# Kernel optimization log

Hardware: AMD Instinct MI355X
Metric: run time of the kernel (lower is better)

The kernel has to match this reference:

```python
import jax, jax.numpy as jnp
import numpy as np

DIM = 128          # per-stream channels (init arg `dim`)
C = 2 * DIM        # fused channels
NH = 8             # num_heads
HD = C // NH       # head_dim = 32
K = 3              # kernel_size
DIL = (2, 3)       # dilation list
ND = len(DIL)
SCALE = HD ** -0.5


def setup_inputs() -> dict:
    key = jax.random.key(0)
    ks = jax.random.split(key, 4)
    B, H, W = 4, 80, 80
    rgb = jax.random.normal(ks[0], (B, DIM, H, W), jnp.float32)
    ir = jax.random.normal(ks[1], (B, DIM, H, W), jnp.float32)
    w_qkv = jax.random.normal(ks[2], (3 * C, C), jnp.float32) * (C ** -0.5)
    w_proj = jax.random.normal(ks[3], (C, C), jnp.float32) * (C ** -0.5)
    b_proj = jnp.zeros((C,), jnp.float32)
    return {"rgb": rgb, "ir": ir, "w_qkv": w_qkv, "w_proj": w_proj, "b_proj": b_proj}


def _unfold(x, k, d):
    # nn.Unfold(k, dilation=d, padding=d*(k-1)//2, stride=1) -> [B, c, k*k, H, W]
    B, c, H, W = x.shape
    p = d * (k - 1) // 2
    xp = jnp.pad(x, ((0, 0), (0, 0), (p, p), (p, p)))
    pats = [xp[:, :, i * d:i * d + H, j * d:j * d + W]
            for i in range(k) for j in range(k)]
    return jnp.stack(pats, axis=2)


def _dilate_attention(q, k, v, d):
    # q,k,v: [B, c, H, W] with c = C // ND; attention over k*k dilated neighborhood
    B, c, H, W = q.shape
    h = c // HD
    N = H * W
    qr = q.reshape(B, h, HD, N)                      # [B,h,hd,N]
    ku = _unfold(k, K, d).reshape(B, h, HD, K * K, N)  # [B,h,hd,K2,N]
    vu = _unfold(v, K, d).reshape(B, h, HD, K * K, N)
    attn = jnp.einsum('bhdn,bhdkn->bhnk', qr, ku) * SCALE   # [B,h,N,K2]
    attn = jax.nn.softmax(attn, axis=-1)
    out = jnp.einsum('bhnk,bhdkn->bnhd', attn, vu)          # head-major channels
    return out.reshape(B, H, W, c)


def reference(rgb, ir, w_qkv, w_proj, b_proj):
    y = jnp.concatenate([rgb, ir], axis=1)            # [B, C, H, W]
    B, Cc, H, W = y.shape
    # 1x1 conv qkv, then split channels as [3, num_dilation, C//num_dilation]
    qkv = jnp.einsum('bchw,oc->bohw', y, w_qkv).reshape(B, 3, ND, Cc // ND, H, W)
    outs = [_dilate_attention(qkv[:, 0, i], qkv[:, 1, i], qkv[:, 2, i], DIL[i])
            for i in range(ND)]
    x = jnp.concatenate(outs, axis=-1)                # [B, H, W, C], dilation-major
    x = x @ w_proj.T + b_proj                         # proj Linear(C, C)
    # residual: add rgb to first half of channels, ir to second half
    return x + y.transpose(0, 2, 3, 1)
```

## Files before the change

### kernel.cpp

```cpp
#include <hip/hip_runtime.h>

#define HH 80
#define WW 80
#define NPIX 6400
#define NB 4
#define BN 25600
#define CDIM 256
#define QKVC 768
#define SCALE 0.17677669529663689f

typedef __attribute__((ext_vector_type(8))) short short8;
typedef __attribute__((ext_vector_type(4))) float floatx4;

__device__ __forceinline__ float b2f(ushort u) {
    return __uint_as_float(((uint)u) << 16);
}
__device__ __forceinline__ ushort f2b(float f) {
    uint u = __float_as_uint(f);
    return (ushort)((u + 0x7fffu + ((u >> 16) & 1u)) >> 16);
}
__device__ __forceinline__ void unpack8(uint4 v, float* f) {
    f[0] = __uint_as_float(v.x << 16); f[1] = __uint_as_float(v.x & 0xffff0000u);
    f[2] = __uint_as_float(v.y << 16); f[3] = __uint_as_float(v.y & 0xffff0000u);
    f[4] = __uint_as_float(v.z << 16); f[5] = __uint_as_float(v.z & 0xffff0000u);
    f[6] = __uint_as_float(v.w << 16); f[7] = __uint_as_float(v.w & 0xffff0000u);
}
__device__ __forceinline__ void gload_lds16(const void* gptr, void* lptr) {
    __builtin_amdgcn_global_load_lds(
        (const __attribute__((address_space(1))) unsigned int*)gptr,
        (__attribute__((address_space(3))) unsigned int*)lptr,
        16, 0, 0);
}

__global__ __launch_bounds__(256) void cast_all_k(
    const float* __restrict__ rgb, const float* __restrict__ ir,
    const float* __restrict__ wq, const float* __restrict__ wp,
    ushort* __restrict__ Yb, ushort* __restrict__ wqb, ushort* __restrict__ wpb)
{
    const int tid = threadIdx.x;
    if (blockIdx.x >= 100) {
        int i = (((blockIdx.x - 100) * 8 + blockIdx.y) * 4 + blockIdx.z) * 256 + tid;
        if (i < QKVC * CDIM) wqb[i] = f2b(wq[i]);
        else                 wpb[i - QKVC * CDIM] = f2b(wp[i - QKVC * CDIM]);
        return;
    }
    __shared__ ushort T[32][72];
    const int pix0 = blockIdx.x * 64;
    const int cb = blockIdx.y;
    const int b = blockIdx.z;

    const int pl = tid & 63, cg = tid >> 6;
    #pragma unroll
    for (int cc = 0; cc < 32; cc += 4) {
        int c = cb * 32 + cc + cg;
        const float* src = (c < 128) ? (rgb + ((size_t)b * 128 + c) * NPIX)
                                     : (ir + ((size_t)b * 128 + (c - 128)) * NPIX);
        T[cc + cg][pl] = f2b(src[pix0 + pl]);
    }
    __syncthreads();
    const int nl = tid >> 2, c0 = (tid & 3) * 8;
    ushort tmp[8];
    #pragma unroll
    for (int j = 0; j < 8; ++j) tmp[j] = T[c0 + j][nl];
    uint4 v;
    v.x = tmp[0] | ((uint)tmp[1] << 16);
    v.y = tmp[2] | ((uint)tmp[3] << 16);
    v.z = tmp[4] | ((uint)tmp[5] << 16);
    v.w = tmp[6] | ((uint)tmp[7] << 16);
    *(uint4*)(&Yb[((size_t)(b * NPIX + pix0 + nl)) * CDIM + cb * 32 + c0]) = v;
}

__device__ __forceinline__ void gemm_nt_body64(
    const ushort* __restrict__ A, const ushort* __restrict__ W,
    ushort* As, ushort* Bs, int n0, int o0, floatx4 acc[4][4])
{
    const int tid = threadIdx.x;
    const int lane = tid & 63;
    const int wave = tid >> 6;
    const int wr = wave >> 1, wc = wave & 1;
    const int l15 = lane & 15, quad = lane >> 4;

    const int srow8 = tid >> 3;
    const int scol  = ((tid & 7) * 8) ^ ((srow8 & 1) << 5);
    const int par   = l15 & 1;

    for (int k0 = 0; k0 < CDIM; k0 += 64) {
        #pragma unroll
        for (int r = 0; r < 4; ++r) {
            const int row = r * 32 + srow8;
            gload_lds16(&A[(size_t)(n0 + row) * CDIM + k0 + scol],
                        As + r * 2048 + wave * 512);
            gload_lds16(&W[(size_t)(o0 + row) * CDIM + k0 + scol],
                        Bs + r * 2048 + wave * 512);
        }
        __syncthreads();
        #pragma unroll
        for (int s = 0; s < 2; ++s) {
            const int fc = ((s ^ par) << 5) + quad * 8;
            short8 af[4], bfr[4];
            #pragma unroll
            for (int i = 0; i < 4; ++i)
                af[i] = *(const short8*)(&As[(wr * 64 + i * 16 + l15) * 64 + fc]);
            #pragma unroll
            for (int j = 0; j < 4; ++j)
                bfr[j] = *(const short8*)(&Bs[(wc * 64 + j * 16 + l15) * 64 + fc]);
            #pragma unroll
            for (int i = 0; i < 4; ++i)
                #pragma unroll
                for (int j = 0; j < 4; ++j)
                    acc[i][j] = __builtin_amdgcn_mfma_f32_16x16x32_bf16(
                        bfr[j], af[i], acc[i][j], 0, 0, 0);
        }
        __syncthreads();
    }
}

__global__ __launch_bounds__(256) void gemm_qkv_mfma(
    const ushort* __restrict__ Yb, const ushort* __restrict__ Wb,
    ushort* __restrict__ qkv2)
{
    __shared__ __align__(16) ushort As[128 * 64];
    __shared__ __align__(16) ushort Bs[128 * 64];
    const int tid = threadIdx.x;
    const int lane = tid & 63;
    const int wave = tid >> 6;
    const int wr = wave >> 1, wc = wave & 1;
    const int l15 = lane & 15, quad = lane >> 4;

    const int bid = blockIdx.x;
    const int swz = (bid & 7) * 150 + (bid >> 3);
    const int n0 = (swz / 6) * 128;
    const int o0 = (swz % 6) * 128;

    floatx4 acc[4][4] = {};
    gemm_nt_body64(Yb, Wb, As, Bs, n0, o0, acc);

    #pragma unroll
    for (int i = 0; i < 4; ++i) {
        const int n = n0 + wr * 64 + i * 16 + l15;
        #pragma unroll
        for (int j = 0; j < 4; ++j) {
            const int o4 = o0 + wc * 64 + j * 16 + quad * 4;
            uint2 v;
            v.x = f2b(acc[i][j][0]) | ((uint)f2b(acc[i][j][1]) << 16);
            v.y = f2b(acc[i][j][2]) | ((uint)f2b(acc[i][j][3]) << 16);
            *(uint2*)(qkv2 + (size_t)(o4 >> 5) * BN * 32 + (size_t)n * 32 + (o4 & 31)) = v;
        }
    }
}

template<int D, bool EDGE>
__device__ __forceinline__ void attn_tile(
    const ushort* __restrict__ qkv2, ushort* __restrict__ X2,
    ushort* kl, int b, int dh, int y0, int x0)
{
    constexpr int RW = 16 + 2 * D;
    constexpr int RP = RW * RW;
    const int tid = threadIdx.x;
    const int lane = tid & 63;
    const int wave = tid >> 6;
    const ushort* Qc = qkv2 + (size_t)dh * BN * 32;
    const ushort* Kc = qkv2 + (size_t)(8 + dh) * BN * 32;
    const ushort* Vc = qkv2 + (size_t)(16 + dh) * BN * 32;

    const int px = tid & 15, py = tid >> 4;
    const int n = b * NPIX + (y0 + py) * WW + (x0 + px);
    float q[32];
    {
        const uint4* qp = (const uint4*)(Qc + (size_t)n * 32);
        uint4 v0 = qp[0], v1 = qp[1], v2 = qp[2], v3 = qp[3];
        unpack8(v0, q); unpack8(v1, q + 8); unpack8(v2, q + 16); unpack8(v3, q + 24);
    }

    #pragma unroll 2
    for (int p0 = 0; p0 < RP; p0 += 64) {
        int p = p0 + lane;
        int ry = p / RW, rx = p % RW;
        int gy = y0 - D + ry, gx = x0 - D + rx;
        if (EDGE) { gy = min(max(gy, 0), HH - 1); gx = min(max(gx, 0), WW - 1); }
        if (p < RP)
            gload_lds16(Kc + (size_t)(b * NPIX + gy * WW + gx) * 32 + wave * 8,
                        kl + (size_t)(wave * RP + p0) * 8);
    }
    __syncthreads();

    float sc[9];
    #pragma unroll
    for (int t = 0; t < 9; ++t) {
        const int dy = t / 3 - 1, dx = t % 3 - 1;
        const int p = (py + D + dy * D) * RW + (px + D + dx * D);
        float s = 0.f;
        bool ok = true;
        if (EDGE) {
            const int yy = y0 + py + dy * D, xx = x0 + px + dx * D;
            ok = (yy >= 0 && yy < HH && xx >= 0 && xx < WW);
        }
        if (ok) {
            #pragma unroll
            for (int c = 0; c < 4; ++c) {
                float kv[8];
                unpack8(*(const uint4*)(kl + (size_t)(c * RP + p) * 8), kv);
                #pragma unroll
                for (int j = 0; j < 8; ++j) s += q[c * 8 + j] * kv[j];
            }
        }
        sc[t] = s * SCALE;
    }
    __syncthreads();

    #pragma unroll 2
    for (int p0 = 0; p0 < RP; p0 += 64) {
        int p = p0 + lane;
        int ry = p / RW, rx = p % RW;
        int gy = y0 - D + ry, gx = x0 - D + rx;
        if (EDGE) { gy = min(max(gy, 0), HH - 1); gx = min(max(gx, 0), WW - 1); }
        if (p < RP)
            gload_lds16(Vc + (size_t)(b * NPIX + gy * WW + gx) * 32 + wave * 8,
                        kl + (size_t)(wave * RP + p0) * 8);
    }

    float m = sc[0];
    #pragma unroll
    for (int t = 1; t < 9; ++t) m = fmaxf(m, sc[t]);
    float sum = 0.f;
    #pragma unroll
    for (int t = 0; t < 9; ++t) { sc[t] = __expf(sc[t] - m); sum += sc[t]; }
    const float inv = 1.f / sum;
    __syncthreads();

    float o[32];
    #pragma unroll
    for (int hd = 0; hd < 32; ++hd) o[hd] = 0.f;
    #pragma unroll
    for (int t = 0; t < 9; ++t) {
        const int dy = t / 3 - 1, dx = t % 3 - 1;
        const int p = (py + D + dy * D) * RW + (px + D + dx * D);
        bool ok = true;
        if (EDGE) {
            const int yy = y0 + py + dy * D, xx = x0 + px + dx * D;
            ok = (yy >= 0 && yy < HH && xx >= 0 && xx < WW);
        }
        if (ok) {
            const float wgt = sc[t] * inv;
            #pragma unroll
            for (int c = 0; c < 4; ++c) {
                float vv[8];
                unpack8(*(const uint4*)(kl + (size_t)(c * RP + p) * 8), vv);
                #pragma unroll
                for (int j = 0; j < 8; ++j) o[c * 8 + j] += wgt * vv[j];
            }
        }
    }
    uint4* xp = (uint4*)(X2 + (size_t)dh * BN * 32 + (size_t)n * 32);
    #pragma unroll
    for (int m4 = 0; m4 < 4; ++m4) {
        uint4 v;
        v.x = f2b(o[8 * m4 + 0]) | ((uint)f2b(o[8 * m4 + 1]) << 16);
        v.y = f2b(o[8 * m4 + 2]) | ((uint)f2b(o[8 * m4 + 3]) << 16);
        v.z = f2b(o[8 * m4 + 4]) | ((uint)f2b(o[8 * m4 + 5]) << 16);
        v.w = f2b(o[8 * m4 + 6]) | ((uint)f2b(o[8 * m4 + 7]) << 16);
        xp[m4] = v;
    }
}

__global__ __launch_bounds__(256) void attn2_k(
    const ushort* __restrict__ qkv2, ushort* __restrict__ X2)
{
    __shared__ __align__(16) ushort kl[4 * 484 * 8];
    const int tile = blockIdx.x;
    const int y0 = (tile / 5) * 16, x0 = (tile % 5) * 16;
    const int dh = blockIdx.y;
    const int b = blockIdx.z;
    const bool inter = (y0 >= 16 && y0 <= 48 && x0 >= 16 && x0 <= 48);
    if (dh < 4) {
        if (inter) attn_tile<2, false>(qkv2, X2, kl, b, dh, y0, x0);
        else       attn_tile<2, true >(qkv2, X2, kl, b, dh, y0, x0);
    } else {
        if (inter) attn_tile<3, false>(qkv2, X2, kl, b, dh, y0, x0);
        else       attn_tile<3, true >(qkv2, X2, kl, b, dh, y0, x0);
    }
}

__global__ __launch_bounds__(256) void proj_mfma(
    const ushort* __restrict__ X2, const ushort* __restrict__ Wpb,
    const float* __restrict__ bp, const ushort* __restrict__ Yb,
    float* __restrict__ out)
{
    __shared__ __align__(16) ushort As[64 * 64];
    __shared__ __align__(16) ushort Bs[128 * 64];
    const int tid = threadIdx.x;
    const int lane = tid & 63;
    const int wave = tid >> 6;
    const int wr = wave >> 1, wc = wave & 1;
    const int l15 = lane & 15, quad = lane >> 4;

    const int bid = blockIdx.x;
    const int swz = (bid & 7) * 100 + (bid >> 3);
    const int n0 = (swz >> 1) * 64;
    const int o0 = (swz & 1) * 128;

    const int srow8 = tid >> 3;
    const int scol  = ((tid & 7) * 8) ^ ((srow8 & 1) << 5);
    const int chunk_sel = ((tid >> 2) & 1) ^ (srow8 & 1);
    const int coff  = (tid & 3) * 8;
    const int par   = l15 & 1;

    floatx4 acc[2][4] = {};

    for (int k0 = 0; k0 < CDIM; k0 += 64) {
        const int cbase = k0 >> 5;
        const ushort* Achunk = X2 + (size_t)(cbase + chunk_sel) * BN * 32;
        #pragma unroll
        for (int r = 0; r < 2; ++r) {
            const int row = r * 32 + srow8;
            gload_lds16(&Achunk[(size_t)(n0 + row) * 32 + coff],
                        As + r * 2048 + wave * 512);
        }
        #pragma unroll
        for (int r = 0; r < 4; ++r) {
            const int row = r * 32 + srow8;
            gload_lds16(&Wpb[(size_t)(o0 + row) * CDIM + k0 + scol],
                        Bs + r * 2048 + wave * 512);
        }
        __syncthreads();
        #pragma unroll
        for (int s = 0; s < 2; ++s) {
            const int fc = ((s ^ par) << 5) + quad * 8;
            short8 af[2], bfr[4];
            #pragma unroll
            for (int i = 0; i < 2; ++i)
                af[i] = *(const short8*)(&As[(wr * 32 + i * 16 + l15) * 64 + fc]);
            #pragma unroll
            for (int j = 0; j < 4; ++j)
                bfr[j] = *(const short8*)(&Bs[(wc * 64 + j * 16 + l15) * 64 + fc]);
            #pragma unroll
            for (int i = 0; i < 2; ++i)
                #pragma unroll
                for (int j = 0; j < 4; ++j)
                    acc[i][j] = __builtin_amdgcn_mfma_f32_16x16x32_bf16(
                        bfr[j], af[i], acc[i][j], 0, 0, 0);
        }
        __syncthreads();
    }

    #pragma unroll
    for (int i = 0; i < 2; ++i) {
        const int n = n0 + wr * 32 + i * 16 + l15;
        #pragma unroll
        for (int j = 0; j < 4; ++j) {
            const int o4 = o0 + wc * 64 + j * 16 + quad * 4;
            const float4 bias = *(const float4*)(bp + o4);
            const ushort4 res = *(const ushort4*)(Yb + (size_t)n * CDIM + o4);
            float4 v;
            v.x = acc[i][j][0] + bias.x + b2f(res.x);
            v.y = acc[i][j][1] + bias.y + b2f(res.y);
            v.z = acc[i][j][2] + bias.z + b2f(res.z);
            v.w = acc[i][j][3] + bias.w + b2f(res.w);
            *(float4*)(out + (size_t)n * CDIM + o4) = v;
        }
    }
}

extern "C" void kernel_launch(void* const* d_in, const int* in_sizes, int n_in,
                              void* d_out, int out_size, void* d_ws, size_t ws_size,
                              hipStream_t stream) {
    const float* rgb    = (const float*)d_in[0];
    const float* ir     = (const float*)d_in[1];
    const float* w_qkv  = (const float*)d_in[2];
    const float* w_proj = (const float*)d_in[3];
    const float* b_proj = (const float*)d_in[4];
    float* out = (float*)d_out;

    ushort* qkv2 = (ushort*)d_ws;
    ushort* Yb   = qkv2 + (size_t)24 * BN * 32;
    ushort* X2   = Yb + (size_t)BN * CDIM;
    ushort* Wqb  = X2 + (size_t)8 * BN * 32;
    ushort* Wpb  = Wqb + (size_t)QKVC * CDIM;

    cast_all_k<<<dim3(132, 8, NB), 256, 0, stream>>>(rgb, ir, w_qkv, w_proj,
                                                     Yb, Wqb, Wpb);
    gemm_qkv_mfma<<<dim3(1200), 256, 0, stream>>>(Yb, Wqb, qkv2);
    attn2_k<<<dim3(25, 8, NB), 256, 0, stream>>>(qkv2, X2);
    proj_mfma<<<dim3(800), 256, 0, stream>>>(X2, Wpb, b_proj, Yb, out);
}
```

Baseline: 135.6 us.

## Replace LDS halo staging in attention with direct per-pixel global loads

The attention kernel no longer stages K and V halo tiles into shared memory with barriers. Each thread now reads its nine neighbour K and V vectors straight from global memory and relies on the cache for reuse. The grid is also flattened so that the eight dilation-heads of a tile run in consecutive blocks, which should improve L2 locality. This drops the barriers and LDS traffic and should let more blocks fit per CU, at the cost of redundant global and cache reads.

```diff
diff --git a/kernel.cpp b/kernel.cpp
--- a/kernel.cpp
+++ b/kernel.cpp
@@ -150,21 +150,18 @@
 }
 
 template<int D, bool EDGE>
-__device__ __forceinline__ void attn_tile(
+__device__ __forceinline__ void attn_px(
     const ushort* __restrict__ qkv2, ushort* __restrict__ X2,
-    ushort* kl, int b, int dh, int y0, int x0)
-{
-    constexpr int RW = 16 + 2 * D;
-    constexpr int RP = RW * RW;
-    const int tid = threadIdx.x;
-    const int lane = tid & 63;
-    const int wave = tid >> 6;
+    int b, int dh, int y0, int x0)
+{
+    const int tid = threadIdx.x;
+    const int px = tid & 15, py = tid >> 4;
+    const int yy0 = y0 + py, xx0 = x0 + px;
+    const int n = b * NPIX + yy0 * WW + xx0;
     const ushort* Qc = qkv2 + (size_t)dh * BN * 32;
     const ushort* Kc = qkv2 + (size_t)(8 + dh) * BN * 32;
     const ushort* Vc = qkv2 + (size_t)(16 + dh) * BN * 32;
 
-    const int px = tid & 15, py = tid >> 4;
-    const int n = b * NPIX + (y0 + py) * WW + (x0 + px);
     float q[32];
     {
         const uint4* qp = (const uint4*)(Qc + (size_t)n * 32);
@@ -172,51 +169,25 @@
         unpack8(v0, q); unpack8(v1, q + 8); unpack8(v2, q + 16); unpack8(v3, q + 24);
     }
 
-    #pragma unroll 2
-    for (int p0 = 0; p0 < RP; p0 += 64) {
-        int p = p0 + lane;
-        int ry = p / RW, rx = p % RW;
-        int gy = y0 - D + ry, gx = x0 - D + rx;
-        if (EDGE) { gy = min(max(gy, 0), HH - 1); gx = min(max(gx, 0), WW - 1); }
-        if (p < RP)
-            gload_lds16(Kc + (size_t)(b * NPIX + gy * WW + gx) * 32 + wave * 8,
-                        kl + (size_t)(wave * RP + p0) * 8);
-    }
-    __syncthreads();
-
     float sc[9];
     #pragma unroll
     for (int t = 0; t < 9; ++t) {
         const int dy = t / 3 - 1, dx = t % 3 - 1;
-        const int p = (py + D + dy * D) * RW + (px + D + dx * D);
-        float s = 0.f;
+        int yy = yy0 + dy * D, xx = xx0 + dx * D;
         bool ok = true;
         if (EDGE) {
-            const int yy = y0 + py + dy * D, xx = x0 + px + dx * D;
             ok = (yy >= 0 && yy < HH && xx >= 0 && xx < WW);
-        }
-        if (ok) {
-            #pragma unroll
-            for (int c = 0; c < 4; ++c) {
-                float kv[8];
-                unpack8(*(const uint4*)(kl + (size_t)(c * RP + p) * 8), kv);
-                #pragma unroll
-                for (int j = 0; j < 8; ++j) s += q[c * 8 + j] * kv[j];
-            }
-        }
-        sc[t] = s * SCALE;
-    }
-    __syncthreads();
-
-    #pragma unroll 2
-    for (int p0 = 0; p0 < RP; p0 += 64) {
-        int p = p0 + lane;
-        int ry = p / RW, rx = p % RW;
-        int gy = y0 - D + ry, gx = x0 - D + rx;
-        if (EDGE) { gy = min(max(gy, 0), HH - 1); gx = min(max(gx, 0), WW - 1); }
-        if (p < RP)
-            gload_lds16(Vc + (size_t)(b * NPIX + gy * WW + gx) * 32 + wave * 8,
-                        kl + (size_t)(wave * RP + p0) * 8);
+            yy = min(max(yy, 0), HH - 1);
+            xx = min(max(xx, 0), WW - 1);
+        }
+        const uint4* kp = (const uint4*)(Kc + (size_t)(b * NPIX + yy * WW + xx) * 32);
+        uint4 k0 = kp[0], k1 = kp[1], k2 = kp[2], k3 = kp[3];
+        float kv[32];
+        unpack8(k0, kv); unpack8(k1, kv + 8); unpack8(k2, kv + 16); unpack8(k3, kv + 24);
+        float s = 0.f;
+        #pragma unroll
+        for (int j = 0; j < 32; ++j) s += q[j] * kv[j];
+        sc[t] = (EDGE && !ok) ? 0.f : s * SCALE;
     }
 
     float m = sc[0];
@@ -226,31 +197,29 @@
     #pragma unroll
     for (int t = 0; t < 9; ++t) { sc[t] = __expf(sc[t] - m); sum += sc[t]; }
     const float inv = 1.f / sum;
-    __syncthreads();
 
     float o[32];
     #pragma unroll
-    for (int hd = 0; hd < 32; ++hd) o[hd] = 0.f;
+    for (int j = 0; j < 32; ++j) o[j] = 0.f;
     #pragma unroll
     for (int t = 0; t < 9; ++t) {
         const int dy = t / 3 - 1, dx = t % 3 - 1;
-        const int p = (py + D + dy * D) * RW + (px + D + dx * D);
+        int yy = yy0 + dy * D, xx = xx0 + dx * D;
         bool ok = true;
         if (EDGE) {
-            const int yy = y0 + py + dy * D, xx = x0 + px + dx * D;
             ok = (yy >= 0 && yy < HH && xx >= 0 && xx < WW);
-        }
-        if (ok) {
-            const float wgt = sc[t] * inv;
-            #pragma unroll
-            for (int c = 0; c < 4; ++c) {
-                float vv[8];
-                unpack8(*(const uint4*)(kl + (size_t)(c * RP + p) * 8), vv);
-                #pragma unroll
-                for (int j = 0; j < 8; ++j) o[c * 8 + j] += wgt * vv[j];
-            }
-        }
-    }
+            yy = min(max(yy, 0), HH - 1);
+            xx = min(max(xx, 0), WW - 1);
+        }
+        const uint4* vp = (const uint4*)(Vc + (size_t)(b * NPIX + yy * WW + xx) * 32);
+        uint4 v0 = vp[0], v1 = vp[1], v2 = vp[2], v3 = vp[3];
+        float vv[32];
+        unpack8(v0, vv); unpack8(v1, vv + 8); unpack8(v2, vv + 16); unpack8(v3, vv + 24);
+        const float wgt = (EDGE && !ok) ? 0.f : sc[t] * inv;
+        #pragma unroll
+        for (int j = 0; j < 32; ++j) o[j] += wgt * vv[j];
+    }
+
     uint4* xp = (uint4*)(X2 + (size_t)dh * BN * 32 + (size_t)n * 32);
     #pragma unroll
     for (int m4 = 0; m4 < 4; ++m4) {
@@ -266,18 +235,19 @@
 __global__ __launch_bounds__(256) void attn2_k(
     const ushort* __restrict__ qkv2, ushort* __restrict__ X2)
 {
-    __shared__ __align__(16) ushort kl[4 * 484 * 8];
-    const int tile = blockIdx.x;
+    const int bid = blockIdx.x;
+    const int dh  = bid & 7;
+    const int t2  = bid >> 3;
+    const int b   = t2 / 25;
+    const int tile = t2 % 25;
     const int y0 = (tile / 5) * 16, x0 = (tile % 5) * 16;
-    const int dh = blockIdx.y;
-    const int b = blockIdx.z;
     const bool inter = (y0 >= 16 && y0 <= 48 && x0 >= 16 && x0 <= 48);
     if (dh < 4) {
-        if (inter) attn_tile<2, false>(qkv2, X2, kl, b, dh, y0, x0);
-        else       attn_tile<2, true >(qkv2, X2, kl, b, dh, y0, x0);
+        if (inter) attn_px<2, false>(qkv2, X2, b, dh, y0, x0);
+        else       attn_px<2, true >(qkv2, X2, b, dh, y0, x0);
     } else {
-        if (inter) attn_tile<3, false>(qkv2, X2, kl, b, dh, y0, x0);
-        else       attn_tile<3, true >(qkv2, X2, kl, b, dh, y0, x0);
+        if (inter) attn_px<3, false>(qkv2, X2, b, dh, y0, x0);
+        else       attn_px<3, true >(qkv2, X2, b, dh, y0, x0);
     }
 }
 
@@ -380,6 +350,6 @@
     cast_all_k<<<dim3(132, 8, NB), 256, 0, stream>>>(rgb, ir, w_qkv, w_proj,
                                                      Yb, Wqb, Wpb);
     gemm_qkv_mfma<<<dim3(1200), 256, 0, stream>>>(Yb, Wqb, qkv2);
-    attn2_k<<<dim3(25, 8, NB), 256, 0, stream>>>(qkv2, X2);
+    attn2_k<<<dim3(800), 256, 0, stream>>>(qkv2, X2);
     proj_mfma<<<dim3(800), 256, 0, stream>>>(X2, Wpb, b_proj, Yb, out);
 }
```

After: 140.2 us. 3.4% more time.
